# Optimization experiments

Measured on AMD Instinct MI355X. Metric: run time of the kernel, lower is better.

Reference implementation:

```python
import jax, jax.numpy as jnp
import numpy as np

EPS = 1e-5

def layernorm(x, g, b):
    mu = jnp.mean(x, axis=-1, keepdims=True)
    var = jnp.mean((x - mu) ** 2, axis=-1, keepdims=True)
    return (x - mu) / jnp.sqrt(var + EPS) * g + b


def setup_inputs() -> dict:
    T, N, H, D = 128, 512, 512, 128
    key = jax.random.key(0)
    ks = jax.random.split(key, 12)
    obs = jax.random.normal(ks[0], (T * N, D), dtype=jnp.float32)
    hx = jax.random.normal(ks[1], (N, 1, H), dtype=jnp.float32)
    on_reset = (jax.random.uniform(ks[2], (T * N, 1)) > 0.02).astype(jnp.float32)
    sc_d = 1.0 / np.sqrt(D)
    sc_h = 1.0 / np.sqrt(H)
    return {
        "obs": obs,
        "hx": hx,
        "on_reset": on_reset,
        "W1": jax.random.normal(ks[3], (H, D), dtype=jnp.float32) * sc_d,
        "b1": jnp.zeros((H,), jnp.float32),
        "g1": jnp.ones((H,), jnp.float32),
        "be1": jnp.zeros((H,), jnp.float32),
        "W2": jax.random.normal(ks[4], (H, H), dtype=jnp.float32) * sc_h,
        "b2": jnp.zeros((H,), jnp.float32),
        "g2": jnp.ones((H,), jnp.float32),
        "be2": jnp.zeros((H,), jnp.float32),
        "Wih": jax.random.normal(ks[5], (3 * H, H), dtype=jnp.float32) * sc_h,
        "Whh": jax.random.normal(ks[6], (3 * H, H), dtype=jnp.float32) * sc_h,
        "bih": jnp.zeros((3 * H,), jnp.float32),
        "bhh": jnp.zeros((3 * H,), jnp.float32),
        "gr": jnp.ones((H,), jnp.float32),
        "br": jnp.zeros((H,), jnp.float32),
    }


def reference(obs, hx, on_reset, W1, b1, g1, be1, W2, b2, g2, be2,
              Wih, Whh, bih, bhh, gr, br):
    N, L, H = hx.shape  # num_rnn_layers L == 1
    T = obs.shape[0] // N
    # dense MLP: Linear -> ReLU -> LayerNorm, twice
    f = layernorm(jax.nn.relu(obs @ W1.T + b1), g1, be1)
    f = layernorm(jax.nn.relu(f @ W2.T + b2), g2, be2)
    x = f.reshape(T, N, H)
    m = on_reset.reshape(T, N, 1)
    # precompute input-to-hidden gates for all timesteps: [T, N, 3H]
    gi = x @ Wih.T + bih
    h0 = hx[:, 0, :]  # [N, H]

    def step(h, inp):
        gi_t, m_t = inp
        h = h * m_t  # auto-reset: zero hidden state at episode boundaries
        gh = h @ Whh.T + bhh
        ir, iz, inn = jnp.split(gi_t, 3, axis=-1)
        hr, hz, hn = jnp.split(gh, 3, axis=-1)
        r = jax.nn.sigmoid(ir + hr)
        z = jax.nn.sigmoid(iz + hz)
        n = jnp.tanh(inn + r * hn)
        h = (1.0 - z) * n + z * h
        return h, h

    hT, ys = jax.lax.scan(step, h0, (gi, m))
    out = layernorm(ys.reshape(T * N, H), gr, br)
    return out, hT[None]  # hx returned as [num_layers, N, H], as in torch multi-step branch
```

## Files before the change

### kernel.cpp

```cpp
#include <hip/hip_runtime.h>
#include <hip/hip_bf16.h>

using bf16 = __hip_bfloat16;
typedef __attribute__((ext_vector_type(8))) short short8;
typedef __attribute__((ext_vector_type(4))) float f32x4;
typedef __attribute__((ext_vector_type(4))) unsigned int u32x4;

static __device__ __forceinline__ float b2f(unsigned short s) {
    unsigned u = ((unsigned)s) << 16;
    return __builtin_bit_cast(float, u);
}
static __device__ __forceinline__ short f2b(float f) {
    __hip_bfloat16 h = __float2bfloat16(f);
    return __builtin_bit_cast(short, h);
}
static __device__ __forceinline__ void load_lds16(const void* g, void* l) {
    __builtin_amdgcn_global_load_lds(
        (const __attribute__((address_space(1))) void*)g,
        (__attribute__((address_space(3))) void*)l, 16, 0, 0);
}

__global__ void f32_to_bf16_vec(const float* __restrict__ in, bf16* __restrict__ out, int n8) {
    int i = blockIdx.x * blockDim.x + threadIdx.x;
    if (i >= n8) return;
    const f32x4* p = (const f32x4*)(in + (size_t)i * 8);
    f32x4 a = p[0], b = p[1];
    short8 o;
    o[0] = f2b(a[0]); o[1] = f2b(a[1]); o[2] = f2b(a[2]); o[3] = f2b(a[3]);
    o[4] = f2b(b[0]); o[5] = f2b(b[1]); o[6] = f2b(b[2]); o[7] = f2b(b[3]);
    *(short8*)(out + (size_t)i * 8) = o;
}

template<int K, bool CONV>
__global__ __launch_bounds__(512, 2) void gemm_ln_fused(
    const void* __restrict__ Xv, const bf16* __restrict__ W,
    const float* __restrict__ bias, const float* __restrict__ g,
    const float* __restrict__ be, bf16* __restrict__ Y)
{
    __shared__ char As[8192];
    __shared__ char Bs[32768];
    __shared__ float lnS[128][4];
    __shared__ float lnQ[128][4];

    const int tid = threadIdx.x;
    const int wv = tid >> 6, lane = tid & 63;
    const int wr = wv >> 2, wc = wv & 3;
    const long Mbase = (long)blockIdx.x * 128;
    const int lc = lane & 15, kgq = lane >> 4;

    f32x4 acc[4][8];
#pragma unroll
    for (int mt = 0; mt < 4; ++mt)
#pragma unroll
        for (int nt = 0; nt < 8; ++nt) acc[mt][nt] = (f32x4){0.f, 0.f, 0.f, 0.f};

    const int rowA_ = tid >> 2, granA_ = tid & 3;

    for (int kb = 0; kb < K / 32; ++kb) {
        __syncthreads();
        {
            const int sb = (granA_ * 16) ^ (((rowA_ >> 1) & 3) << 4);
            if (CONV) {
                const float* Xf = (const float*)Xv;
                const float* src = Xf + (Mbase + rowA_) * K + kb * 32 + sb / 2;
                f32x4 a0 = *(const f32x4*)src;
                f32x4 a1 = *(const f32x4*)(src + 4);
                short8 o;
                o[0] = f2b(a0[0]); o[1] = f2b(a0[1]); o[2] = f2b(a0[2]); o[3] = f2b(a0[3]);
                o[4] = f2b(a1[0]); o[5] = f2b(a1[1]); o[6] = f2b(a1[2]); o[7] = f2b(a1[3]);
                *(short8*)(As + rowA_ * 64 + granA_ * 16) = o;
            } else {
                const bf16* X = (const bf16*)Xv;
                load_lds16((const char*)X + ((Mbase + rowA_) * K + kb * 32) * 2 + sb,
                           As + tid * 16);
            }
        }
#pragma unroll
        for (int j = 0; j < 4; ++j) {
            const int idx = j * 512 + tid;
            const int row = idx >> 2, gran = idx & 3;
            const int sb = (gran * 16) ^ (((row >> 1) & 3) << 4);
            load_lds16((const char*)W + ((long)row * K + kb * 32) * 2 + sb,
                       Bs + idx * 16);
        }
        __syncthreads();

        short8 a[4], b[8];
#pragma unroll
        for (int mt = 0; mt < 4; ++mt) {
            const int ar = wr * 64 + mt * 16 + lc;
            a[mt] = *(const short8*)(As + ar * 64 + ((kgq * 16) ^ (((ar >> 1) & 3) << 4)));
        }
#pragma unroll
        for (int nt = 0; nt < 8; ++nt) {
            const int br = wc * 128 + nt * 16 + lc;
            b[nt] = *(const short8*)(Bs + br * 64 + ((kgq * 16) ^ (((br >> 1) & 3) << 4)));
        }
#pragma unroll
        for (int mt = 0; mt < 4; ++mt)
#pragma unroll
            for (int nt = 0; nt < 8; ++nt)
                acc[mt][nt] = __builtin_amdgcn_mfma_f32_16x16x32_bf16(a[mt], b[nt], acc[mt][nt], 0, 0, 0);
    }

    float bcol[8];
#pragma unroll
    for (int nt = 0; nt < 8; ++nt) bcol[nt] = bias[wc * 128 + nt * 16 + lc];

    float sp[4][4], qp[4][4];
#pragma unroll
    for (int mt = 0; mt < 4; ++mt)
#pragma unroll
        for (int r = 0; r < 4; ++r) { sp[mt][r] = 0.f; qp[mt][r] = 0.f; }
#pragma unroll
    for (int mt = 0; mt < 4; ++mt)
#pragma unroll
        for (int nt = 0; nt < 8; ++nt)
#pragma unroll
            for (int r = 0; r < 4; ++r) {
                float v = fmaxf(acc[mt][nt][r] + bcol[nt], 0.f);
                acc[mt][nt][r] = v;
                sp[mt][r] += v; qp[mt][r] += v * v;
            }
#pragma unroll
    for (int m = 1; m < 16; m <<= 1)
#pragma unroll
        for (int mt = 0; mt < 4; ++mt)
#pragma unroll
            for (int r = 0; r < 4; ++r) {
                sp[mt][r] += __shfl_xor(sp[mt][r], m);
                qp[mt][r] += __shfl_xor(qp[mt][r], m);
            }
    if (lc == 0) {
#pragma unroll
        for (int mt = 0; mt < 4; ++mt)
#pragma unroll
            for (int r = 0; r < 4; ++r) {
                const int grow = wr * 64 + mt * 16 + kgq * 4 + r;
                lnS[grow][wc] = sp[mt][r];
                lnQ[grow][wc] = qp[mt][r];
            }
    }
    __syncthreads();

    float gcol[8], becol[8];
#pragma unroll
    for (int nt = 0; nt < 8; ++nt) {
        const int col = wc * 128 + nt * 16 + lc;
        gcol[nt] = g[col]; becol[nt] = be[col];
    }
#pragma unroll
    for (int mt = 0; mt < 4; ++mt)
#pragma unroll
        for (int r = 0; r < 4; ++r) {
            const int grow = wr * 64 + mt * 16 + kgq * 4 + r;
            f32x4 vs = *(const f32x4*)&lnS[grow][0];
            f32x4 vq = *(const f32x4*)&lnQ[grow][0];
            const float s = vs[0] + vs[1] + vs[2] + vs[3];
            const float q = vq[0] + vq[1] + vq[2] + vq[3];
            const float mu   = s * (1.f / 512.f);
            const float var  = q * (1.f / 512.f) - mu * mu;
            const float rstd = rsqrtf(var + 1e-5f);
            bf16* yrow = Y + (Mbase + grow) * 512;
#pragma unroll
            for (int nt = 0; nt < 8; ++nt) {
                const int col = wc * 128 + nt * 16 + lc;
                yrow[col] = __float2bfloat16((acc[mt][nt][r] - mu) * rstd * gcol[nt] + becol[nt]);
            }
        }
}

template<int K, bool RELU>
__global__ __launch_bounds__(256) void gemm_xwt(
    const bf16* __restrict__ X, const bf16* __restrict__ W,
    const float* __restrict__ bias, bf16* __restrict__ C, int Nout)
{
    __shared__ char As[8192];
    __shared__ char Bs[8192];
    const int tid  = threadIdx.x;
    const int wave = tid >> 6, lane = tid & 63;
    const int wr = wave >> 1, wc = wave & 1;
    const long Mbase = (long)blockIdx.y * 128;
    const int  Nbase = blockIdx.x * 128;
    const int lc = lane & 15, kgq = lane >> 4;

    f32x4 acc[4][4];
#pragma unroll
    for (int i = 0; i < 4; ++i)
#pragma unroll
        for (int j = 0; j < 4; ++j) acc[i][j] = (f32x4){0.f, 0.f, 0.f, 0.f};

    const int row0_ = tid >> 2, gran_ = tid & 3;

    for (int kb = 0; kb < K / 32; ++kb) {
        __syncthreads();
#pragma unroll
        for (int q = 0; q < 2; ++q) {
            const int idx = q * 256 + tid;
            const int row = q * 64 + row0_;
            const int sb = (gran_ * 16) ^ (((row >> 1) & 3) << 4);
            load_lds16((const char*)X + ((Mbase + row) * K + kb * 32) * 2 + sb,
                       As + idx * 16);
            load_lds16((const char*)W + ((long)(Nbase + row) * K + kb * 32) * 2 + sb,
                       Bs + idx * 16);
        }
        __syncthreads();

        short8 a[4], b[4];
#pragma unroll
        for (int mt = 0; mt < 4; ++mt) {
            const int ar = wr * 64 + mt * 16 + lc;
            a[mt] = *(const short8*)(As + ar * 64 + ((kgq * 16) ^ (((ar >> 1) & 3) << 4)));
        }
#pragma unroll
        for (int nt = 0; nt < 4; ++nt) {
            const int br = wc * 64 + nt * 16 + lc;
            b[nt] = *(const short8*)(Bs + br * 64 + ((kgq * 16) ^ (((br >> 1) & 3) << 4)));
        }
#pragma unroll
        for (int mt = 0; mt < 4; ++mt)
#pragma unroll
            for (int nt = 0; nt < 4; ++nt)
                acc[mt][nt] = __builtin_amdgcn_mfma_f32_16x16x32_bf16(a[mt], b[nt], acc[mt][nt], 0, 0, 0);
    }

#pragma unroll
    for (int mt = 0; mt < 4; ++mt) {
        int row0 = wr * 64 + mt * 16 + (lane >> 4) * 4;
#pragma unroll
        for (int nt = 0; nt < 4; ++nt) {
            int col = Nbase + wc * 64 + nt * 16 + (lane & 15);
            float bv = bias[col];
#pragma unroll
            for (int r = 0; r < 4; ++r) {
                float v = acc[mt][nt][r] + bv;
                if (RELU) v = fmaxf(v, 0.f);
                C[(Mbase + row0 + r) * (long)Nout + col] = __float2bfloat16(v);
            }
        }
    }
}

__global__ __launch_bounds__(256) void ln_rows512_f32out(
    const bf16* __restrict__ in, float* __restrict__ out,
    const float* __restrict__ g, const float* __restrict__ be)
{
    const int lane = threadIdx.x & 63;
    const long row = (long)blockIdx.x * 4 + (threadIdx.x >> 6);
    const bf16* rp = in + row * 512;
    short8 v = *(const short8*)&rp[lane * 8];
    float x[8]; float s = 0.f, sq = 0.f;
#pragma unroll
    for (int j = 0; j < 8; ++j) { x[j] = b2f((unsigned short)v[j]); s += x[j]; sq += x[j] * x[j]; }
#pragma unroll
    for (int m = 1; m < 64; m <<= 1) { s += __shfl_xor(s, m); sq += __shfl_xor(sq, m); }
    float mu   = s * (1.f / 512.f);
    float var  = sq * (1.f / 512.f) - mu * mu;
    float rstd = rsqrtf(var + 1e-5f);
    float* op = out + row * 512 + lane * 8;
#pragma unroll
    for (int c4 = 0; c4 < 2; ++c4) {
        f32x4 o;
#pragma unroll
        for (int j = 0; j < 4; ++j) {
            int c = lane * 8 + c4 * 4 + j;
            o[j] = (x[c4 * 4 + j] - mu) * rstd * g[c] + be[c];
        }
        *(f32x4*)(op + c4 * 4) = o;
    }
}

__global__ __launch_bounds__(256, 1) void gru_scan14(
    const bf16* __restrict__ gi, const float* __restrict__ on_reset,
    const float* __restrict__ hx, const bf16* __restrict__ Whh,
    const float* __restrict__ bhh,
    bf16* __restrict__ hA, bf16* __restrict__ hB,
    bf16* __restrict__ h_all, float* __restrict__ hT,
    unsigned* __restrict__ bar)
{
    __shared__ bf16 Wl[96 * 512];
    __shared__ bf16 hS[32 * 512];

    const int tid = threadIdx.x;
    const int bid = blockIdx.x;
    const int xcd = bid & 7, sub = bid >> 3;
    const int g   = xcd * 2 + (sub & 1);
    const int cc  = sub >> 1;
    const int n0 = g * 32, c0 = cc * 32;
    unsigned* gflags = bar + g * 512;
    unsigned* myflag = gflags + cc * 32;

    const int w = tid >> 6, lane = tid & 63;
    const int lc = lane & 15, kg = lane >> 4;
    const int rt = w >> 1, hh = w & 1;
    const int cg = c0 + hh * 16 + lc;

    char* Wlb = (char*)Wl;
    char* hSb = (char*)hS;

    {
        const char* Wb = (const char*)Whh;
#pragma unroll
        for (int i2 = 0; i2 < 24; ++i2) {
            const int i = i2 * 256 + tid;
            const int row = i >> 6, l16 = i & 63;
            const int gRow = (row >> 5) * 512 + c0 + (row & 31);
            load_lds16(Wb + (size_t)gRow * 1024 + ((l16 * 16) ^ ((row & 7) << 4)),
                       Wlb + i * 16);
        }
    }

    const float bhr = bhh[cg], bhz = bhh[512 + cg], bhn = bhh[1024 + cg];

    float hreg[4];
#pragma unroll
    for (int r = 0; r < 4; ++r) {
        const int row = rt * 16 + kg * 4 + r;
        const float m0 = on_reset[n0 + row];
        float v = hx[(size_t)(n0 + row) * 512 + cg];
        hreg[r] = v;
        hA[(size_t)(n0 + row) * 512 + cg] = __float2bfloat16(v * m0);
    }
    __syncthreads();
    asm volatile("s_waitcnt vmcnt(0)" ::: "memory");
    if (tid == 0)
        __hip_atomic_store(myflag, 1u, __ATOMIC_RELEASE, __HIP_MEMORY_SCOPE_AGENT);

#pragma unroll 1
    for (int t = 0; t < 128; ++t) {
        const bf16* hcur = (t & 1) ? hB : hA;
        bf16*       hnxt = (t & 1) ? hA : hB;

        float irv[4], izv[4], inv_[4], mcur[4], mnx[4];
#pragma unroll
        for (int r = 0; r < 4; ++r) {
            const int row = rt * 16 + kg * 4 + r;
            const unsigned short* gp =
                (const unsigned short*)gi + ((size_t)t * 512 + n0 + row) * 1536;
            irv[r]  = b2f(__builtin_nontemporal_load(gp + cg));
            izv[r]  = b2f(__builtin_nontemporal_load(gp + 512 + cg));
            inv_[r] = b2f(__builtin_nontemporal_load(gp + 1024 + cg));
            mcur[r] = on_reset[(size_t)t * 512 + n0 + row];
            mnx[r]  = (t < 127) ? on_reset[(size_t)(t + 1) * 512 + n0 + row] : 1.f;
        }

        if (w == 0) {
            const unsigned tgt = (unsigned)(t + 1);
            const unsigned* fp = gflags + (lane & 15) * 32;
            for (;;) {
                unsigned v = tgt;
                if (lane < 16) {
                    asm volatile("global_load_dword %0, %1, off sc0 sc1\n\t"
                                 "s_waitcnt vmcnt(0)"
                                 : "=v"(v) : "v"(fp) : "memory");
                }
                if (__all(v >= tgt)) break;
                __builtin_amdgcn_s_sleep(2);
            }
        }
        __syncthreads();

        {
            const char* hbp = (const char*)hcur + (size_t)n0 * 1024;
            u32x4 hv[8];
#pragma unroll
            for (int j = 0; j < 8; ++j) {
                const int i = j * 256 + tid;
                const int row = i >> 6, l16 = i & 63;
                const char* src = hbp + row * 1024 + l16 * 16;
                asm volatile("global_load_dwordx4 %0, %1, off sc0 sc1"
                             : "=v"(hv[j]) : "v"(src));
            }
            asm volatile("s_waitcnt vmcnt(0)" ::: "memory");
            __builtin_amdgcn_sched_barrier(0);
#pragma unroll
            for (int j = 0; j < 8; ++j) {
                const int i = j * 256 + tid;
                const int row = i >> 6, l16 = i & 63;
                *(u32x4*)(hSb + row * 1024 + ((l16 * 16) ^ ((row & 7) << 4))) = hv[j];
            }
        }
        __syncthreads();

        short8 aF[16];
        const int arow = rt * 16 + lc;
        const int asw = (arow & 7) << 4;
#pragma unroll
        for (int kc = 0; kc < 16; ++kc)
            aF[kc] = *(const short8*)(hSb + arow * 1024 + ((kc * 64 + kg * 16) ^ asw));

        f32x4 acc[3];
#pragma unroll
        for (int gt = 0; gt < 3; ++gt) acc[gt] = (f32x4){0.f, 0.f, 0.f, 0.f};
#pragma unroll
        for (int gt = 0; gt < 3; ++gt) {
            const int wrow = gt * 32 + hh * 16 + lc;
            const int wsw = (wrow & 7) << 4;
#pragma unroll
            for (int kc = 0; kc < 16; ++kc) {
                short8 bq = *(const short8*)(Wlb + wrow * 1024 + ((kc * 64 + kg * 16) ^ wsw));
                acc[gt] = __builtin_amdgcn_mfma_f32_16x16x32_bf16(aF[kc], bq, acc[gt], 0, 0, 0);
            }
        }

#pragma unroll
        for (int r = 0; r < 4; ++r) {
            const int row = rt * 16 + kg * 4 + r;
            const float hr = acc[0][r] + bhr;
            const float hz = acc[1][r] + bhz;
            const float hn = acc[2][r] + bhn;
            const float rg = 1.f / (1.f + __expf(-(irv[r] + hr)));
            const float zg = 1.f / (1.f + __expf(-(izv[r] + hz)));
            const float e2 = __expf(2.f * (inv_[r] + rg * hn));
            const float ng = 1.f - 2.f / (e2 + 1.f);
            const float hv = (1.f - zg) * ng + zg * (hreg[r] * mcur[r]);
            hreg[r] = hv;
            __builtin_nontemporal_store(
                f2b(hv), (short*)&h_all[((size_t)t * 512 + n0 + row) * 512 + cg]);
            if (t < 127) {
                const unsigned short hb16 = (unsigned short)f2b(hv * mnx[r]);
                const unsigned partner = (unsigned)(unsigned short)__shfl_xor((int)hb16, 1);
                if ((lc & 1) == 0) {
                    const unsigned pk = (unsigned)hb16 | (partner << 16);
                    unsigned* dst = (unsigned*)&hnxt[(size_t)(n0 + row) * 512 + cg];
                    asm volatile("global_store_dword %0, %1, off sc0 sc1"
                                 :: "v"(dst), "v"(pk) : "memory");
                }
            }
        }

        if (t < 127) {
            __syncthreads();
            if (tid == 0) {
                unsigned fv = (unsigned)(t + 2);
                asm volatile("global_store_dword %0, %1, off sc0 sc1"
                             :: "v"(myflag), "v"(fv) : "memory");
            }
        }
    }

#pragma unroll
    for (int r = 0; r < 4; ++r) {
        const int row = rt * 16 + kg * 4 + r;
        hT[(size_t)(n0 + row) * 512 + cg] = hreg[r];
    }
}

extern "C" void kernel_launch(void* const* d_in, const int* in_sizes, int n_in,
                              void* d_out, int out_size, void* d_ws, size_t ws_size,
                              hipStream_t stream) {
    const float* obs      = (const float*)d_in[0];
    const float* hx       = (const float*)d_in[1];
    const float* on_reset = (const float*)d_in[2];
    const float* W1  = (const float*)d_in[3];
    const float* b1  = (const float*)d_in[4];
    const float* g1  = (const float*)d_in[5];
    const float* be1 = (const float*)d_in[6];
    const float* W2  = (const float*)d_in[7];
    const float* b2  = (const float*)d_in[8];
    const float* g2  = (const float*)d_in[9];
    const float* be2 = (const float*)d_in[10];
    const float* Wih = (const float*)d_in[11];
    const float* Whh = (const float*)d_in[12];
    const float* bih = (const float*)d_in[13];
    const float* bhh = (const float*)d_in[14];
    const float* gr  = (const float*)d_in[15];
    const float* br  = (const float*)d_in[16];

    char* ws = (char*)d_ws;
    bf16* W1b  = (bf16*)(ws + 0);
    bf16* W2b  = (bf16*)(ws + 131072);
    bf16* Wihb = (bf16*)(ws + 655360);
    bf16* Whhb = (bf16*)(ws + 2228224);
    bf16* Y2   = (bf16*)(ws + 3801088);
    bf16* GI   = (bf16*)(ws + 3801088 + 67108864);
    bf16* Y1   = GI;
    bf16* hAb  = (bf16*)(ws + 0);
    bf16* hBb  = (bf16*)(ws + 655360);
    unsigned* bar = (unsigned*)(ws + 1179648);
    bf16* h_all = Y2;

    f32_to_bf16_vec<<<(8192 + 255) / 256,  256, 0, stream>>>(W1,  W1b,  8192);
    f32_to_bf16_vec<<<(32768 + 255) / 256, 256, 0, stream>>>(W2,  W2b,  32768);
    f32_to_bf16_vec<<<(98304 + 255) / 256, 256, 0, stream>>>(Wih, Wihb, 98304);
    f32_to_bf16_vec<<<(98304 + 255) / 256, 256, 0, stream>>>(Whh, Whhb, 98304);

    gemm_ln_fused<128, true ><<<512, 512, 0, stream>>>(obs, W1b, b1, g1, be1, Y1);
    gemm_ln_fused<512, false><<<512, 512, 0, stream>>>(Y1,  W2b, b2, g2, be2, Y2);
    gemm_xwt<512, false><<<dim3(12, 512), 256, 0, stream>>>(Y2, Wihb, bih, GI, 1536);

    hipMemsetAsync(bar, 0, 32768, stream);
    float* out_p = (float*)d_out;
    float* hT_p  = out_p + (size_t)65536 * 512;
    gru_scan14<<<256, 256, 0, stream>>>(GI, on_reset, hx, Whhb, bhh,
                                        hAb, hBb, h_all, hT_p, bar);

    ln_rows512_f32out<<<16384, 256, 0, stream>>>(h_all, out_p, gr, br);
}
```

Before: 744.3 us.

## Fuse output LayerNorm into GRU scan using shared-memory hidden-state row stats

The separate LayerNorm kernel is removed. The scan now computes per-row mean and variance from the full hidden-state tile it already stages in shared memory each step, and writes the normalized fp32 output for step t-1 directly, so the bf16 h_all round trip disappears. The reset mask is now applied when the A operand is loaded, zeroing whole rows, rather than being pre-multiplied into the exchanged state. This adds per-step LDS reduction work and a barrier inside the latency-critical serial loop, plus an extra final barrier wait and tile reload to normalize the last step. LayerNorm statistics now come from bf16-rounded hidden values, which may slightly change accuracy.

```diff
diff --git a/kernel.cpp b/kernel.cpp
--- a/kernel.cpp
+++ b/kernel.cpp
@@ -241,45 +241,20 @@
     }
 }
 
-__global__ __launch_bounds__(256) void ln_rows512_f32out(
-    const bf16* __restrict__ in, float* __restrict__ out,
-    const float* __restrict__ g, const float* __restrict__ be)
-{
-    const int lane = threadIdx.x & 63;
-    const long row = (long)blockIdx.x * 4 + (threadIdx.x >> 6);
-    const bf16* rp = in + row * 512;
-    short8 v = *(const short8*)&rp[lane * 8];
-    float x[8]; float s = 0.f, sq = 0.f;
-#pragma unroll
-    for (int j = 0; j < 8; ++j) { x[j] = b2f((unsigned short)v[j]); s += x[j]; sq += x[j] * x[j]; }
-#pragma unroll
-    for (int m = 1; m < 64; m <<= 1) { s += __shfl_xor(s, m); sq += __shfl_xor(sq, m); }
-    float mu   = s * (1.f / 512.f);
-    float var  = sq * (1.f / 512.f) - mu * mu;
-    float rstd = rsqrtf(var + 1e-5f);
-    float* op = out + row * 512 + lane * 8;
-#pragma unroll
-    for (int c4 = 0; c4 < 2; ++c4) {
-        f32x4 o;
-#pragma unroll
-        for (int j = 0; j < 4; ++j) {
-            int c = lane * 8 + c4 * 4 + j;
-            o[j] = (x[c4 * 4 + j] - mu) * rstd * g[c] + be[c];
-        }
-        *(f32x4*)(op + c4 * 4) = o;
-    }
-}
-
-__global__ __launch_bounds__(256, 1) void gru_scan14(
+__global__ __launch_bounds__(256, 1) void gru_scan16(
     const bf16* __restrict__ gi, const float* __restrict__ on_reset,
     const float* __restrict__ hx, const bf16* __restrict__ Whh,
-    const float* __restrict__ bhh,
+    const float* __restrict__ bhh, const float* __restrict__ gr,
+    const float* __restrict__ br,
     bf16* __restrict__ hA, bf16* __restrict__ hB,
-    bf16* __restrict__ h_all, float* __restrict__ hT,
+    float* __restrict__ out, float* __restrict__ hT,
     unsigned* __restrict__ bar)
 {
     __shared__ bf16 Wl[96 * 512];
     __shared__ bf16 hS[32 * 512];
+    __shared__ float mrow[32];
+    __shared__ float lnSs[32];
+    __shared__ float lnQq[32];
 
     const int tid = threadIdx.x;
     const int bid = blockIdx.x;
@@ -311,15 +286,15 @@
     }
 
     const float bhr = bhh[cg], bhz = bhh[512 + cg], bhn = bhh[1024 + cg];
+    const float grg = gr[cg], brb = br[cg];
 
     float hreg[4];
 #pragma unroll
     for (int r = 0; r < 4; ++r) {
         const int row = rt * 16 + kg * 4 + r;
-        const float m0 = on_reset[n0 + row];
         float v = hx[(size_t)(n0 + row) * 512 + cg];
         hreg[r] = v;
-        hA[(size_t)(n0 + row) * 512 + cg] = __float2bfloat16(v * m0);
+        hA[(size_t)(n0 + row) * 512 + cg] = __float2bfloat16(v);
     }
     __syncthreads();
     asm volatile("s_waitcnt vmcnt(0)" ::: "memory");
@@ -331,7 +306,7 @@
         const bf16* hcur = (t & 1) ? hB : hA;
         bf16*       hnxt = (t & 1) ? hA : hB;
 
-        float irv[4], izv[4], inv_[4], mcur[4], mnx[4];
+        float irv[4], izv[4], inv_[4], mcur[4];
 #pragma unroll
         for (int r = 0; r < 4; ++r) {
             const int row = rt * 16 + kg * 4 + r;
@@ -341,8 +316,8 @@
             izv[r]  = b2f(__builtin_nontemporal_load(gp + 512 + cg));
             inv_[r] = b2f(__builtin_nontemporal_load(gp + 1024 + cg));
             mcur[r] = on_reset[(size_t)t * 512 + n0 + row];
-            mnx[r]  = (t < 127) ? on_reset[(size_t)(t + 1) * 512 + n0 + row] : 1.f;
-        }
+        }
+        if (tid < 32) mrow[tid] = on_reset[(size_t)t * 512 + n0 + tid];
 
         if (w == 0) {
             const unsigned tgt = (unsigned)(t + 1);
@@ -385,9 +360,13 @@
         short8 aF[16];
         const int arow = rt * 16 + lc;
         const int asw = (arow & 7) << 4;
-#pragma unroll
-        for (int kc = 0; kc < 16; ++kc)
-            aF[kc] = *(const short8*)(hSb + arow * 1024 + ((kc * 64 + kg * 16) ^ asw));
+        const unsigned mb = (mrow[arow] == 0.f) ? 0u : 0xffffffffu;
+#pragma unroll
+        for (int kc = 0; kc < 16; ++kc) {
+            u32x4 av = *(const u32x4*)(hSb + arow * 1024 + ((kc * 64 + kg * 16) ^ asw));
+            av[0] &= mb; av[1] &= mb; av[2] &= mb; av[3] &= mb;
+            aF[kc] = __builtin_bit_cast(short8, av);
+        }
 
         f32x4 acc[3];
 #pragma unroll
@@ -400,6 +379,39 @@
             for (int kc = 0; kc < 16; ++kc) {
                 short8 bq = *(const short8*)(Wlb + wrow * 1024 + ((kc * 64 + kg * 16) ^ wsw));
                 acc[gt] = __builtin_amdgcn_mfma_f32_16x16x32_bf16(aF[kc], bq, acc[gt], 0, 0, 0);
+            }
+        }
+
+        {
+            const int lrow = tid >> 3, lseg = tid & 7;
+            const int lsw = (lrow & 7) << 4;
+            float s = 0.f, q = 0.f;
+#pragma unroll
+            for (int sgm = 0; sgm < 8; ++sgm) {
+                u32x4 v = *(const u32x4*)(hSb + lrow * 1024 + ((lseg * 128 + sgm * 16) ^ lsw));
+#pragma unroll
+                for (int d = 0; d < 4; ++d) {
+                    float f0 = b2f((unsigned short)(v[d] & 0xffff));
+                    float f1 = b2f((unsigned short)(v[d] >> 16));
+                    s += f0 + f1; q += f0 * f0 + f1 * f1;
+                }
+            }
+#pragma unroll
+            for (int m = 1; m < 8; m <<= 1) { s += __shfl_xor(s, m); q += __shfl_xor(q, m); }
+            if (lseg == 0) { lnSs[lrow] = s; lnQq[lrow] = q; }
+        }
+        __syncthreads();
+
+        if (t > 0) {
+#pragma unroll
+            for (int r = 0; r < 4; ++r) {
+                const int row = rt * 16 + kg * 4 + r;
+                const float mu   = lnSs[row] * (1.f / 512.f);
+                const float var  = lnQq[row] * (1.f / 512.f) - mu * mu;
+                const float rstd = rsqrtf(var + 1e-5f);
+                const float o = (hreg[r] - mu) * rstd * grg + brb;
+                __builtin_nontemporal_store(
+                    o, out + ((size_t)(t - 1) * 512 + n0 + row) * 512 + cg);
             }
         }
 
@@ -415,33 +427,88 @@
             const float ng = 1.f - 2.f / (e2 + 1.f);
             const float hv = (1.f - zg) * ng + zg * (hreg[r] * mcur[r]);
             hreg[r] = hv;
-            __builtin_nontemporal_store(
-                f2b(hv), (short*)&h_all[((size_t)t * 512 + n0 + row) * 512 + cg]);
-            if (t < 127) {
-                const unsigned short hb16 = (unsigned short)f2b(hv * mnx[r]);
-                const unsigned partner = (unsigned)(unsigned short)__shfl_xor((int)hb16, 1);
-                if ((lc & 1) == 0) {
-                    const unsigned pk = (unsigned)hb16 | (partner << 16);
-                    unsigned* dst = (unsigned*)&hnxt[(size_t)(n0 + row) * 512 + cg];
-                    asm volatile("global_store_dword %0, %1, off sc0 sc1"
-                                 :: "v"(dst), "v"(pk) : "memory");
-                }
-            }
-        }
-
-        if (t < 127) {
-            __syncthreads();
-            if (tid == 0) {
-                unsigned fv = (unsigned)(t + 2);
+            const unsigned short hb16 = (unsigned short)f2b(hv);
+            const unsigned partner = (unsigned)(unsigned short)__shfl_xor((int)hb16, 1);
+            if ((lc & 1) == 0) {
+                const unsigned pk = (unsigned)hb16 | (partner << 16);
+                unsigned* dst = (unsigned*)&hnxt[(size_t)(n0 + row) * 512 + cg];
                 asm volatile("global_store_dword %0, %1, off sc0 sc1"
-                             :: "v"(myflag), "v"(fv) : "memory");
-            }
-        }
-    }
-
+                             :: "v"(dst), "v"(pk) : "memory");
+            }
+        }
+
+        __syncthreads();
+        if (tid == 0) {
+            unsigned fv = (unsigned)(t + 2);
+            asm volatile("global_store_dword %0, %1, off sc0 sc1"
+                         :: "v"(myflag), "v"(fv) : "memory");
+        }
+    }
+
+    if (w == 0) {
+        const unsigned tgt = 129u;
+        const unsigned* fp = gflags + (lane & 15) * 32;
+        for (;;) {
+            unsigned v = tgt;
+            if (lane < 16) {
+                asm volatile("global_load_dword %0, %1, off sc0 sc1\n\t"
+                             "s_waitcnt vmcnt(0)"
+                             : "=v"(v) : "v"(fp) : "memory");
+            }
+            if (__all(v >= tgt)) break;
+            __builtin_amdgcn_s_sleep(2);
+        }
+    }
+    __syncthreads();
+    {
+        const bf16* hcur = hA;
+        const char* hbp = (const char*)hcur + (size_t)n0 * 1024;
+        u32x4 hv[8];
+#pragma unroll
+        for (int j = 0; j < 8; ++j) {
+            const int i = j * 256 + tid;
+            const int row = i >> 6, l16 = i & 63;
+            const char* src = hbp + row * 1024 + l16 * 16;
+            asm volatile("global_load_dwordx4 %0, %1, off sc0 sc1"
+                         : "=v"(hv[j]) : "v"(src));
+        }
+        asm volatile("s_waitcnt vmcnt(0)" ::: "memory");
+        __builtin_amdgcn_sched_barrier(0);
+#pragma unroll
+        for (int j = 0; j < 8; ++j) {
+            const int i = j * 256 + tid;
+            const int row = i >> 6, l16 = i & 63;
+            *(u32x4*)(hSb + row * 1024 + ((l16 * 16) ^ ((row & 7) << 4))) = hv[j];
+        }
+    }
+    __syncthreads();
+    {
+        const int lrow = tid >> 3, lseg = tid & 7;
+        const int lsw = (lrow & 7) << 4;
+        float s = 0.f, q = 0.f;
+#pragma unroll
+        for (int sgm = 0; sgm < 8; ++sgm) {
+            u32x4 v = *(const u32x4*)(hSb + lrow * 1024 + ((lseg * 128 + sgm * 16) ^ lsw));
+#pragma unroll
+            for (int d = 0; d < 4; ++d) {
+                float f0 = b2f((unsigned short)(v[d] & 0xffff));
+                float f1 = b2f((unsigned short)(v[d] >> 16));
+                s += f0 + f1; q += f0 * f0 + f1 * f1;
+            }
+        }
+#pragma unroll
+        for (int m = 1; m < 8; m <<= 1) { s += __shfl_xor(s, m); q += __shfl_xor(q, m); }
+        if (lseg == 0) { lnSs[lrow] = s; lnQq[lrow] = q; }
+    }
+    __syncthreads();
 #pragma unroll
     for (int r = 0; r < 4; ++r) {
         const int row = rt * 16 + kg * 4 + r;
+        const float mu   = lnSs[row] * (1.f / 512.f);
+        const float var  = lnQq[row] * (1.f / 512.f) - mu * mu;
+        const float rstd = rsqrtf(var + 1e-5f);
+        const float o = (hreg[r] - mu) * rstd * grg + brb;
+        __builtin_nontemporal_store(o, out + ((size_t)127 * 512 + n0 + row) * 512 + cg);
         hT[(size_t)(n0 + row) * 512 + cg] = hreg[r];
     }
 }
@@ -478,7 +545,6 @@
     bf16* hAb  = (bf16*)(ws + 0);
     bf16* hBb  = (bf16*)(ws + 655360);
     unsigned* bar = (unsigned*)(ws + 1179648);
-    bf16* h_all = Y2;
 
     f32_to_bf16_vec<<<(8192 + 255) / 256,  256, 0, stream>>>(W1,  W1b,  8192);
     f32_to_bf16_vec<<<(32768 + 255) / 256, 256, 0, stream>>>(W2,  W2b,  32768);
@@ -492,8 +558,6 @@
     hipMemsetAsync(bar, 0, 32768, stream);
     float* out_p = (float*)d_out;
     float* hT_p  = out_p + (size_t)65536 * 512;
-    gru_scan14<<<256, 256, 0, stream>>>(GI, on_reset, hx, Whhb, bhh,
-                                        hAb, hBb, h_all, hT_p, bar);
-
-    ln_rows512_f32out<<<16384, 256, 0, stream>>>(h_all, out_p, gr, br);
-}
+    gru_scan16<<<256, 256, 0, stream>>>(GI, on_reset, hx, Whhb, bhh, gr, br,
+                                        hAb, hBb, out_p, hT_p, bar);
+}
```

After: 906.2 us. 21.8% more time.
